# Performance work log

Hardware: AMD Instinct MI355X
Metric: run time of the kernel (lower is better)

## Reference

```python
import jax, jax.numpy as jnp
from jax import lax
import numpy as np

V, E, H = 27, 64, 128
B, S_ENC, S_DEC = 256, 512, 512


def _simple_rnn(x_emb, Wx, Wh, b, h0):
    """Keras SimpleRNN: h_t = tanh(x_t @ Wx + h_{t-1} @ Wh + b).
    x_emb: [B, S, E]; returns (outputs [B, S, H], last state [B, H])."""
    # Precompute input projections for all timesteps (one big GEMM).
    xw = jnp.einsum('bse,eh->bsh', x_emb, Wx) + b  # [B, S, H]

    def step(h, xw_t):
        h = jnp.tanh(xw_t + h @ Wh)
        return h, h

    h_last, hs = lax.scan(step, h0, jnp.swapaxes(xw, 0, 1))  # scan over time
    return jnp.swapaxes(hs, 0, 1), h_last


def setup_inputs() -> dict:
    key = jax.random.key(0)
    ks = jax.random.split(key, 8)
    s = lambda fan_in: 1.0 / np.sqrt(fan_in)
    return {
        'enc_ids': jax.random.randint(ks[0], (B, S_ENC), 0, V, dtype=jnp.int32),
        'dec_ids': jax.random.randint(ks[1], (B, S_DEC), 0, V, dtype=jnp.int32),
        'embed':  jax.random.normal(ks[2], (V, E), jnp.float32) * 0.05,
        'enc_Wx': jax.random.normal(ks[3], (E, H), jnp.float32) * s(E),
        'enc_Wh': jax.random.normal(ks[4], (H, H), jnp.float32) * s(H),
        'enc_b':  jnp.zeros((H,), jnp.float32),
        'dec_Wx': jax.random.normal(ks[5], (E, H), jnp.float32) * s(E),
        'dec_Wh': jax.random.normal(ks[6], (H, H), jnp.float32) * s(H),
        'dec_b':  jnp.zeros((H,), jnp.float32),
        'dense_W': jax.random.normal(ks[7], (H, V), jnp.float32) * s(H),
        'dense_b': jnp.zeros((V,), jnp.float32),
    }


def reference(enc_ids, dec_ids, embed, enc_Wx, enc_Wh, enc_b,
              dec_Wx, dec_Wh, dec_b, dense_W, dense_b):
    enc_emb = embed[enc_ids]                      # [B, S_enc, E]
    h0 = jnp.zeros((enc_ids.shape[0], H), embed.dtype)
    _, enc_state = _simple_rnn(enc_emb, enc_Wx, enc_Wh, enc_b, h0)
    dec_emb = embed[dec_ids]                      # [B, S_dec, E]
    dec_out, _ = _simple_rnn(dec_emb, dec_Wx, dec_Wh, dec_b, enc_state)
    logits = jnp.einsum('bsh,hv->bsv', dec_out, dense_W) + dense_b
    return logits
```

## Files before the change

### kernel.cpp

```cpp
#include <hip/hip_runtime.h>

#define V_ 27
#define E_ 64
#define H_ 128
#define S_ 512
#define SCL 2.8853900817779268f

typedef float f32x2 __attribute__((ext_vector_type(2)));
typedef float f32x4 __attribute__((ext_vector_type(4)));

#define BAR() asm volatile("s_waitcnt lgkmcnt(0)\n\ts_barrier" ::: "memory")

#if __has_builtin(__builtin_elementwise_fma)
#define EFMA(H2, W2, A) (A) = __builtin_elementwise_fma((f32x2)(H2), (f32x2)(W2), (A))
#else
#define EFMA(H2, W2, A) do { f32x2 _h = (H2), _w = (W2); \
    (A).x = fmaf(_h.x, _w.x, (A).x); (A).y = fmaf(_h.y, _w.y, (A).y); } while (0)
#endif
#define LO2(Q) __builtin_shufflevector((Q), (Q), 0, 1)
#define HI2(Q) __builtin_shufflevector((Q), (Q), 2, 3)

#define PINW() asm volatile("" : "+v"(WA[0]), "+v"(WA[1]), "+v"(WA[2]), "+v"(WA[3]), \
                                 "+v"(WA[4]), "+v"(WA[5]), "+v"(WA[6]), "+v"(WA[7]), \
                                 "+v"(WB[0]), "+v"(WB[1]), "+v"(WB[2]), "+v"(WB[3]), \
                                 "+v"(WB[4]), "+v"(WB[5]), "+v"(WB[6]), "+v"(WB[7]))
#define PIND() asm volatile("" : "+v"(DQ[0]), "+v"(DQ[1]), "+v"(DQ[2]), "+v"(DQ[3]))

template<int CTRL>
__device__ __forceinline__ float dpp_add(float x) {
    int y = __builtin_amdgcn_update_dpp(0, __builtin_bit_cast(int, x), CTRL, 0xF, 0xF, true);
    return x + __builtin_bit_cast(float, y);
}
#define QP_1032 0xB1
#define QP_2301 0x4E
#define RR8 0x128

__device__ __forceinline__ float tanh_ps(float P) {
#if __has_builtin(__builtin_amdgcn_exp2f)
    float e = __builtin_amdgcn_exp2f(P);
#else
    float e = __expf(P * 0.69314718055994531f);
#endif
#if __has_builtin(__builtin_amdgcn_rcpf)
    float q = __builtin_amdgcn_rcpf(e + 1.0f);
    return fmaf(-2.0f, q, 1.0f);
#else
    return 1.0f - __fdividef(2.0f, e + 1.0f);
#endif
}

__global__ void prep_T(const float* __restrict__ embed,
                       const float* __restrict__ eWx, const float* __restrict__ eb,
                       const float* __restrict__ dWx, const float* __restrict__ db_,
                       float* __restrict__ Tg) {
    int tbl = blockIdx.x / V_;
    int v   = blockIdx.x - tbl * V_;
    int j   = threadIdx.x;
    const float* Wx = tbl ? dWx : eWx;
    const float* bb = tbl ? db_ : eb;
    float s = bb[j];
    #pragma unroll
    for (int e = 0; e < E_; ++e) s = fmaf(embed[v * E_ + e], Wx[e * H_ + j], s);
    Tg[tbl * V_ * H_ + v * H_ + j] = s * SCL;
}

#define LOADW(WH) do {                                                   \
    _Pragma("unroll")                                                    \
    for (int i = 0; i < 8; ++i) {                                        \
        const float* _a = (WH) + (16 * kk + 2 * i) * H_ + j0;            \
        f32x4 ra = *(const f32x4*)(_a);                                  \
        f32x4 rb = *(const f32x4*)(_a + H_);                             \
        WA[i] = (f32x4){ra.x * SCL, rb.x * SCL, ra.y * SCL, rb.y * SCL}; \
        WB[i] = (f32x4){ra.z * SCL, rb.z * SCL, ra.w * SCL, rb.w * SCL}; \
    }                                                                    \
} while (0)

#define ACCP(HP, I) do { f32x2 _hp = (HP);              \
    EFMA(_hp, LO2(WA[I]), P0); EFMA(_hp, HI2(WA[I]), P1); \
    EFMA(_hp, LO2(WB[I]), P2); EFMA(_hp, HI2(WB[I]), P3); } while (0)

#define RNN_STEP(WBUF, DENSEF, LOADPAIRF, IDP, TLB, DOSTORE, OUTP) do {             \
    PINW();                                                                         \
    if (DENSEF) PIND();                                                             \
    f32x2 P0 = {0,0}, P1 = {0,0}, P2 = {0,0}, P3 = {0,0};                           \
    ACCP(LO2(HA), 0); ACCP(HI2(HA), 1); ACCP(LO2(HB), 2); ACCP(HI2(HB), 3);         \
    ACCP(LO2(HC), 4); ACCP(HI2(HC), 5); ACCP(LO2(HD), 6); ACCP(HI2(HD), 7);         \
    float s0 = P0.x + P0.y, s1 = P1.x + P1.y;                                       \
    float s2 = P2.x + P2.y, s3 = P3.x + P3.y;                                       \
    s0 = dpp_add<QP_2301>(dpp_add<QP_1032>(s0));                                    \
    s1 = dpp_add<QP_2301>(dpp_add<QP_1032>(s1));                                    \
    s2 = dpp_add<QP_2301>(dpp_add<QP_1032>(s2));                                    \
    s3 = dpp_add<QP_2301>(dpp_add<QP_1032>(s3));                                    \
    float s01 = c1 ? s1 : s0;                                                       \
    float s23 = c1 ? s3 : s2;                                                       \
    float r   = c2 ? s23 : s01;                                                     \
    r = dpp_add<RR8>(r);                                        \
    float hnew = tanh_ps(r + Tv);                                                   \
    if (wrlane) (WBUF)[wrword] = hnew;          \
    BAR();                                                                          \
    const f32x4* hbp = (const f32x4*)((WBUF) + 20 * kk);                            \
    f32x4 N0 = hbp[0], N1 = hbp[1], N2 = hbp[2], N3 = hbp[3];     \
    float Tv_n = (TLB)[id_next * H_ + jd];                        \
    int2 idpr_n = idpr;                                                             \
    if (LOADPAIRF) idpr_n = *(const int2*)((IDP) + 2);      \
    if (DENSEF) {                                            \
        f32x2 E0 = {0,0}, E1 = {0,0};                                               \
        EFMA(LO2(HA), LO2(DQ[0]), E0); EFMA(HI2(HA), HI2(DQ[0]), E1);               \
        EFMA(LO2(HB), LO2(DQ[1]), E0); EFMA(HI2(HB), HI2(DQ[1]), E1);               \
        EFMA(LO2(HC), LO2(DQ[2]), E0); EFMA(HI2(HC), HI2(DQ[2]), E1);               \
        EFMA(LO2(HD), LO2(DQ[3]), E0); EFMA(HI2(HD), HI2(DQ[3]), E1);               \
        f32x2 E = E0 + E1;                                                          \
        float d = E.x + E.y;                                                        \
        d = dpp_add<RR8>(dpp_add<QP_2301>(dpp_add<QP_1032>(d)));                    \
        if (DOSTORE) (OUTP)[0] = d + db;                   \
    }                                                                               \
    HA = N0; HB = N1; HC = N2; HD = N3;                                             \
    if (LOADPAIRF) { idpr = idpr_n; id_next = idpr_n.x; }                           \
    else           { id_next = idpr.y; }                                            \
    Tv = Tv_n;                                                                      \
} while (0)

__global__ __attribute__((amdgpu_flat_work_group_size(256, 256), amdgpu_waves_per_eu(1, 1)))
void seq2seq_rnn_kernel(const int* __restrict__ enc_ids, const int* __restrict__ dec_ids,
                        const float* __restrict__ enc_Wh, const float* __restrict__ dec_Wh,
                        const float* __restrict__ dense_W, const float* __restrict__ dense_b,
                        const float* __restrict__ Tg,
                        float* __restrict__ out) {
    __shared__ __align__(16) float lds_h0[160];
    __shared__ __align__(16) float lds_h1[160];
    __shared__ __align__(16) int   lds_ids[2 * S_ + 2];
    __shared__ __align__(16) float lds_T[2 * V_ * H_];

    const int tid  = threadIdx.x;
    const int b    = blockIdx.x;
    const int lane = tid & 63;
    const int w    = tid >> 6;
    const int kk   = (lane & 3) | (((lane >> 3) & 1) << 2);
    const int jl   = ((lane >> 2) & 1) | (((lane >> 4) & 3) << 1);
    const int j0     = (w << 5) + (jl << 2);
    const int jd     = j0 + (lane & 3);
    const int wrword = 20 * (jd >> 4) + (jd & 15);
    const bool wrlane = (lane & 8) == 0;
    const bool c1 = (lane & 1) != 0;
    const bool c2 = (lane & 2) != 0;
    const int vd   = (w << 3) | jl;

    if (tid < 128) ((int4*)lds_ids)[tid] = ((const int4*)(enc_ids + b * S_))[tid];
    else ((int4*)(lds_ids + S_))[tid - 128] = ((const int4*)(dec_ids + b * S_))[tid - 128];
    if (tid < 2) lds_ids[2 * S_ + tid] = 0;
    #pragma unroll
    for (int i = 0; i < 7; ++i) {
        int idx = tid + 256 * i;
        if (idx < 2 * V_ * H_ / 4) ((f32x4*)lds_T)[idx] = ((const f32x4*)Tg)[idx];
    }
    if (tid < 160) lds_h0[tid] = 0.0f;

    f32x4 WA[8], WB[8];
    LOADW(enc_Wh);

    f32x4 DQ[4]; float db = 0.0f;
    {
        int vc = (vd < V_) ? vd : 0;
        const float* dp = dense_W + (16 * kk) * V_ + vc;
        DQ[0] = (f32x4){dp[ 0 * V_], dp[ 1 * V_], dp[ 2 * V_], dp[ 3 * V_]};
        DQ[1] = (f32x4){dp[ 4 * V_], dp[ 5 * V_], dp[ 6 * V_], dp[ 7 * V_]};
        DQ[2] = (f32x4){dp[ 8 * V_], dp[ 9 * V_], dp[10 * V_], dp[11 * V_]};
        DQ[3] = (f32x4){dp[12 * V_], dp[13 * V_], dp[14 * V_], dp[15 * V_]};
        if (vd < V_) db = dense_b[vd];
    }
    const bool dlane = ((lane & 11) == 0) && (vd < V_);
    float* outd = out + b * (S_ * V_) + vd;
    __syncthreads();

    f32x4 HA, HB, HC, HD;
    {
        const f32x4* hbp = (const f32x4*)(lds_h0 + 20 * kk);
        HA = hbp[0]; HB = hbp[1]; HC = hbp[2]; HD = hbp[3];
    }

    {
        int2  idpr = make_int2(0, 0);
        int   id_next = lds_ids[1];
        float Tv      = lds_T[lds_ids[0] * H_ + jd];
        for (int t = 0; t < S_; t += 2) {
            RNN_STEP(lds_h1, false, true,  lds_ids + t, lds_T, false, (float*)out);
            RNN_STEP(lds_h0, false, false, lds_ids + t, lds_T, false, (float*)out);
        }
    }

    LOADW(dec_Wh);

    {
        const int*   ids_d = lds_ids + S_;
        float*       Td    = lds_T + V_ * H_;
        int2  idpr = make_int2(0, 0);
        int   id_next = ids_d[1];
        float Tv      = Td[ids_d[0] * H_ + jd];
        for (int t = 0; t < S_; t += 2) {
            RNN_STEP(lds_h1, true, true,  ids_d + t, Td,
                     dlane && (t > 0), outd + (t - 1) * V_);
            RNN_STEP(lds_h0, true, false, ids_d + t, Td,
                     dlane, outd + t * V_);
        }
    }

    {
        f32x2 E0 = {0,0}, E1 = {0,0};
        EFMA(LO2(HA), LO2(DQ[0]), E0); EFMA(HI2(HA), HI2(DQ[0]), E1);
        EFMA(LO2(HB), LO2(DQ[1]), E0); EFMA(HI2(HB), HI2(DQ[1]), E1);
        EFMA(LO2(HC), LO2(DQ[2]), E0); EFMA(HI2(HC), HI2(DQ[2]), E1);
        EFMA(LO2(HD), LO2(DQ[3]), E0); EFMA(HI2(HD), HI2(DQ[3]), E1);
        f32x2 E = E0 + E1;
        float d = E.x + E.y;
        d = dpp_add<RR8>(dpp_add<QP_2301>(dpp_add<QP_1032>(d)));
        if (dlane) outd[(S_ - 1) * V_] = d + db;
    }
}

extern "C" void kernel_launch(void* const* d_in, const int* in_sizes, int n_in,
                              void* d_out, int out_size, void* d_ws, size_t ws_size,
                              hipStream_t stream) {
    const int*   enc_ids = (const int*)d_in[0];
    const int*   dec_ids = (const int*)d_in[1];
    const float* embed   = (const float*)d_in[2];
    const float* enc_Wx  = (const float*)d_in[3];
    const float* enc_Wh  = (const float*)d_in[4];
    const float* enc_b   = (const float*)d_in[5];
    const float* dec_Wx  = (const float*)d_in[6];
    const float* dec_Wh  = (const float*)d_in[7];
    const float* dec_b   = (const float*)d_in[8];
    const float* dense_W = (const float*)d_in[9];
    const float* dense_b = (const float*)d_in[10];
    float* out = (float*)d_out;
    float* Tg  = (float*)d_ws;

    hipLaunchKernelGGL(prep_T, dim3(2 * V_), dim3(H_), 0, stream,
                       embed, enc_Wx, enc_b, dec_Wx, dec_b, Tg);
    hipLaunchKernelGGL(seq2seq_rnn_kernel, dim3(256), dim3(256), 0, stream,
                       enc_ids, dec_ids, enc_Wh, dec_Wh, dense_W, dense_b, Tg, out);
}
```

Measured before the change: 330.3 us.

## Fuse embedding-projection table build into the RNN kernel, drop prep launch

Removes the separate prep_T kernel and has each block compute the per-vocab input projection table directly into LDS. Each thread holds one column of Wx in registers and loops over the 27 vocab entries. This drops a kernel launch and the global round trip for the table. In exchange, every one of the 256 blocks redundantly does about 27x64 FMAs per thread in its prologue. The per-step id prefetch also becomes a single scalar LDS load in place of the int2 pair scheme.

Result: slower. 358.6 us (+8.6%).

```diff
diff --git a/kernel.cpp b/kernel.cpp
--- a/kernel.cpp
+++ b/kernel.cpp
@@ -49,21 +49,6 @@
 #endif
 }
 
-__global__ void prep_T(const float* __restrict__ embed,
-                       const float* __restrict__ eWx, const float* __restrict__ eb,
-                       const float* __restrict__ dWx, const float* __restrict__ db_,
-                       float* __restrict__ Tg) {
-    int tbl = blockIdx.x / V_;
-    int v   = blockIdx.x - tbl * V_;
-    int j   = threadIdx.x;
-    const float* Wx = tbl ? dWx : eWx;
-    const float* bb = tbl ? db_ : eb;
-    float s = bb[j];
-    #pragma unroll
-    for (int e = 0; e < E_; ++e) s = fmaf(embed[v * E_ + e], Wx[e * H_ + j], s);
-    Tg[tbl * V_ * H_ + v * H_ + j] = s * SCL;
-}
-
 #define LOADW(WH) do {                                                   \
     _Pragma("unroll")                                                    \
     for (int i = 0; i < 8; ++i) {                                        \
@@ -79,7 +64,7 @@
     EFMA(_hp, LO2(WA[I]), P0); EFMA(_hp, HI2(WA[I]), P1); \
     EFMA(_hp, LO2(WB[I]), P2); EFMA(_hp, HI2(WB[I]), P3); } while (0)
 
-#define RNN_STEP(WBUF, DENSEF, LOADPAIRF, IDP, TLB, DOSTORE, OUTP) do {             \
+#define RNN_STEP(WBUF, DENSEF, IDP2, TLB, DOSTORE, OUTP) do {                       \
     PINW();                                                                         \
     if (DENSEF) PIND();                                                             \
     f32x2 P0 = {0,0}, P1 = {0,0}, P2 = {0,0}, P3 = {0,0};                           \
@@ -101,8 +86,7 @@
     const f32x4* hbp = (const f32x4*)((WBUF) + 20 * kk);                            \
     f32x4 N0 = hbp[0], N1 = hbp[1], N2 = hbp[2], N3 = hbp[3];     \
     float Tv_n = (TLB)[id_next * H_ + jd];                        \
-    int2 idpr_n = idpr;                                                             \
-    if (LOADPAIRF) idpr_n = *(const int2*)((IDP) + 2);      \
+    int   id_n2 = (IDP2)[0];                                    \
     if (DENSEF) {                                            \
         f32x2 E0 = {0,0}, E1 = {0,0};                                               \
         EFMA(LO2(HA), LO2(DQ[0]), E0); EFMA(HI2(HA), HI2(DQ[0]), E1);               \
@@ -115,16 +99,17 @@
         if (DOSTORE) (OUTP)[0] = d + db;                   \
     }                                                                               \
     HA = N0; HB = N1; HC = N2; HD = N3;                                             \
-    if (LOADPAIRF) { idpr = idpr_n; id_next = idpr_n.x; }                           \
-    else           { id_next = idpr.y; }                                            \
+    id_next = id_n2;                                                                \
     Tv = Tv_n;                                                                      \
 } while (0)
 
 __global__ __attribute__((amdgpu_flat_work_group_size(256, 256), amdgpu_waves_per_eu(1, 1)))
 void seq2seq_rnn_kernel(const int* __restrict__ enc_ids, const int* __restrict__ dec_ids,
-                        const float* __restrict__ enc_Wh, const float* __restrict__ dec_Wh,
+                        const float* __restrict__ embed,
+                        const float* __restrict__ enc_Wx, const float* __restrict__ enc_b,
+                        const float* __restrict__ enc_Wh, const float* __restrict__ dec_Wx,
+                        const float* __restrict__ dec_b,  const float* __restrict__ dec_Wh,
                         const float* __restrict__ dense_W, const float* __restrict__ dense_b,
-                        const float* __restrict__ Tg,
                         float* __restrict__ out) {
     __shared__ __align__(16) float lds_h0[160];
     __shared__ __align__(16) float lds_h1[160];
@@ -148,12 +133,24 @@
     if (tid < 128) ((int4*)lds_ids)[tid] = ((const int4*)(enc_ids + b * S_))[tid];
     else ((int4*)(lds_ids + S_))[tid - 128] = ((const int4*)(dec_ids + b * S_))[tid - 128];
     if (tid < 2) lds_ids[2 * S_ + tid] = 0;
-    #pragma unroll
-    for (int i = 0; i < 7; ++i) {
-        int idx = tid + 256 * i;
-        if (idx < 2 * V_ * H_ / 4) ((f32x4*)lds_T)[idx] = ((const f32x4*)Tg)[idx];
-    }
     if (tid < 160) lds_h0[tid] = 0.0f;
+
+    {
+        const int   jT  = tid & 127;
+        const float* Wx = (tid < 128) ? enc_Wx : dec_Wx;
+        const float* bb = (tid < 128) ? enc_b  : dec_b;
+        float* Tdst = lds_T + (tid >> 7) * (V_ * H_) + jT;
+        float wx[E_];
+        #pragma unroll
+        for (int e = 0; e < E_; ++e) wx[e] = Wx[e * H_ + jT];
+        float bj = bb[jT];
+        for (int v = 0; v < V_; ++v) {
+            float s = bj;
+            #pragma unroll
+            for (int e = 0; e < E_; ++e) s = fmaf(embed[v * E_ + e], wx[e], s);
+            Tdst[v * H_] = s * SCL;
+        }
+    }
 
     f32x4 WA[8], WB[8];
     LOADW(enc_Wh);
@@ -179,27 +176,25 @@
     }
 
     {
-        int2  idpr = make_int2(0, 0);
         int   id_next = lds_ids[1];
         float Tv      = lds_T[lds_ids[0] * H_ + jd];
         for (int t = 0; t < S_; t += 2) {
-            RNN_STEP(lds_h1, false, true,  lds_ids + t, lds_T, false, (float*)out);
-            RNN_STEP(lds_h0, false, false, lds_ids + t, lds_T, false, (float*)out);
+            RNN_STEP(lds_h1, false, lds_ids + t + 2, lds_T, false, (float*)out);
+            RNN_STEP(lds_h0, false, lds_ids + t + 3, lds_T, false, (float*)out);
         }
     }
 
     LOADW(dec_Wh);
 
     {
-        const int*   ids_d = lds_ids + S_;
-        float*       Td    = lds_T + V_ * H_;
-        int2  idpr = make_int2(0, 0);
+        const int* ids_d = lds_ids + S_;
+        float*     Td    = lds_T + V_ * H_;
         int   id_next = ids_d[1];
         float Tv      = Td[ids_d[0] * H_ + jd];
         for (int t = 0; t < S_; t += 2) {
-            RNN_STEP(lds_h1, true, true,  ids_d + t, Td,
+            RNN_STEP(lds_h1, true, ids_d + t + 2, Td,
                      dlane && (t > 0), outd + (t - 1) * V_);
-            RNN_STEP(lds_h0, true, false, ids_d + t, Td,
+            RNN_STEP(lds_h0, true, ids_d + t + 3, Td,
                      dlane, outd + t * V_);
         }
     }
@@ -232,10 +227,8 @@
     const float* dense_W = (const float*)d_in[9];
     const float* dense_b = (const float*)d_in[10];
     float* out = (float*)d_out;
-    float* Tg  = (float*)d_ws;
-
-    hipLaunchKernelGGL(prep_T, dim3(2 * V_), dim3(H_), 0, stream,
-                       embed, enc_Wx, enc_b, dec_Wx, dec_b, Tg);
+
     hipLaunchKernelGGL(seq2seq_rnn_kernel, dim3(256), dim3(256), 0, stream,
-                       enc_ids, dec_ids, enc_Wh, dec_Wh, dense_W, dense_b, Tg, out);
-}
+                       enc_ids, dec_ids, embed, enc_Wx, enc_b, enc_Wh,
+                       dec_Wx, dec_b, dec_Wh, dense_W, dense_b, out);
+}
```
